# Kernel tuning notes

Hardware: AMD Instinct MI355X
Metric: run time of the kernel (lower is better)

The kernel has to match this reference:

```python
import jax, jax.numpy as jnp
import numpy as np

N_NODES = 131072
N_EDGES = 2097152
IN_DIM = 768
HID = 64
NODES_PER_GRAPH = 32
OUT_DIM = 2


def setup_inputs() -> dict:
    key = jax.random.key(0)
    k1, k2, k3, k4 = jax.random.split(key, 4)
    x = jax.random.normal(k1, (N_NODES, IN_DIM), dtype=jnp.float32)
    edge_index = jax.random.randint(k2, (2, N_EDGES), 0, N_NODES, dtype=jnp.int64)
    W_conv = jax.random.normal(k3, (IN_DIM, HID), dtype=jnp.float32) * 0.02
    b_conv = jnp.zeros((HID,), dtype=jnp.float32)
    W_lin = jax.random.normal(k4, (OUT_DIM, HID * NODES_PER_GRAPH), dtype=jnp.float32) * 0.02
    b_lin = jnp.zeros((OUT_DIM,), dtype=jnp.float32)
    return {"x": x, "edge_index": edge_index, "W_conv": W_conv,
            "b_conv": b_conv, "W_lin": W_lin, "b_lin": b_lin}


def reference(x, edge_index, W_conv, b_conv, W_lin, b_lin):
    N = x.shape[0]
    # GCNConv: add self-loops, symmetric normalization D^-1/2 (A+I) D^-1/2
    loops = jnp.arange(N, dtype=edge_index.dtype)
    src = jnp.concatenate([edge_index[0], loops])  # [E+N]
    dst = jnp.concatenate([edge_index[1], loops])
    deg = jax.ops.segment_sum(jnp.ones_like(dst, dtype=x.dtype), dst, num_segments=N)
    dinv = jax.lax.rsqrt(deg)  # deg >= 1 due to self-loops
    norm = dinv[src] * dinv[dst]  # [E+N]
    h = x @ W_conv  # [N, HID]
    msg = h[src] * norm[:, None]  # gather + scale
    out = jax.ops.segment_sum(msg, dst, num_segments=N) + b_conv  # scatter-add
    out = jax.nn.relu(out)
    out = out.reshape(-1, HID * NODES_PER_GRAPH)  # [B, 2048]
    logits = out @ W_lin.T + b_lin  # [B, OUT_DIM]
    return jax.nn.log_softmax(logits, axis=1)
```

## Files before the change

### kernel.cpp

```cpp
#include <hip/hip_runtime.h>
#include <hip/hip_bf16.h>

#define N_NODES 131072
#define N_EDGES 2097152
#define IN_DIM 768
#define HID 64
#define NPG 32
#define NGRAPH (N_NODES / NPG)

#define BM 128
#define GEMM_BLOCKS (N_NODES / BM)

#define RNG 128
#define NB (N_NODES / RNG)
#define EPB 4096
#define NCB (N_EDGES / EPB)
#define PBLK 8
#define RPB (NCB / PBLK)
#define PREP_BLK 192

typedef __attribute__((ext_vector_type(8))) short bf16x8;
typedef __attribute__((ext_vector_type(4))) float f32x4;

static __device__ __forceinline__ unsigned short f2bf(float f) {
    __hip_bfloat16 h = __float2bfloat16(f);
    return *reinterpret_cast<unsigned short*>(&h);
}
static __device__ __forceinline__ float bf2f(unsigned short s) {
    return __uint_as_float(((unsigned int)s) << 16);
}

__global__ __launch_bounds__(256) void gcn_prep_count(const float* __restrict__ W,
                                                      unsigned short* __restrict__ Wt,
                                                      const int* __restrict__ dst,
                                                      unsigned int* __restrict__ C) {
    __shared__ unsigned int hist[NB];
    int tid = threadIdx.x;
    if (blockIdx.x < PREP_BLK) {
        int i = blockIdx.x * 256 + tid;
        if (i < IN_DIM * HID) {
            int k = i >> 6, n = i & 63;
            Wt[n * IN_DIM + k] = f2bf(W[i]);
        }
        return;
    }
    int cb = blockIdx.x - PREP_BLK;
    for (int t = tid; t < NB; t += 256) hist[t] = 0u;
    __syncthreads();
    int base = cb * EPB;
    #pragma unroll
    for (int u = 0; u < EPB / 256; ++u) {
        int d = dst[base + u * 256 + tid];
        atomicAdd(&hist[d >> 7], 1u);
    }
    __syncthreads();
    for (int t = tid; t < NB; t += 256) C[(size_t)cb * NB + t] = hist[t];
}

__global__ __launch_bounds__(256) void gcn_prefA(unsigned int* __restrict__ C,
                                                 unsigned int* __restrict__ S) {
    int tid = threadIdx.x;
    int p = blockIdx.x;
    #pragma unroll
    for (int c = 0; c < 4; ++c) {
        int t = tid + c * 256;
        unsigned int run = 0;
        for (int r = 0; r < RPB; r += 8) {
            unsigned int v[8];
            size_t base = ((size_t)(p * RPB + r)) * NB + t;
            #pragma unroll
            for (int j = 0; j < 8; ++j) v[j] = C[base + (size_t)j * NB];
            #pragma unroll
            for (int j = 0; j < 8; ++j) { C[base + (size_t)j * NB] = run; run += v[j]; }
        }
        S[p * NB + t] = run;
    }
}

__global__ __launch_bounds__(256) void gcn_prefB(unsigned int* __restrict__ S,
                                                 unsigned int* __restrict__ bstart) {
    __shared__ unsigned int sm[256];
    int tid = threadIdx.x;
    unsigned int lexcl[4];
    unsigned int lrun = 0;
    #pragma unroll
    for (int j = 0; j < 4; ++j) {
        unsigned int t = tid * 4 + j;
        unsigned int r = 0;
        #pragma unroll
        for (int p = 0; p < PBLK; ++p) {
            unsigned int v = S[p * NB + t];
            S[p * NB + t] = r;
            r += v;
        }
        lexcl[j] = lrun;
        lrun += r;
    }
    sm[tid] = lrun;
    __syncthreads();
    for (int off = 1; off < 256; off <<= 1) {
        unsigned int u = (tid >= off) ? sm[tid - off] : 0u;
        __syncthreads();
        sm[tid] += u;
        __syncthreads();
    }
    unsigned int texcl = sm[tid] - lrun;
    #pragma unroll
    for (int j = 0; j < 4; ++j) bstart[tid * 4 + j] = texcl + lexcl[j];
    if (tid == 255) bstart[NB] = N_EDGES;
}

__global__ __launch_bounds__(256) void gcn_scatter(const int* __restrict__ src,
                                                   const int* __restrict__ dst,
                                                   const unsigned int* __restrict__ C,
                                                   const unsigned int* __restrict__ S,
                                                   const unsigned int* __restrict__ bstart,
                                                   unsigned int* __restrict__ part) {
    __shared__ unsigned int off[NB];
    int tid = threadIdx.x, cb = blockIdx.x;
    int p = cb >> 6;
    for (int t = tid; t < NB; t += 256)
        off[t] = bstart[t] + S[p * NB + t] + C[(size_t)cb * NB + t];
    __syncthreads();
    int base = cb * EPB;
    #pragma unroll
    for (int u = 0; u < EPB / 256; ++u) {
        int i = base + u * 256 + tid;
        int d = dst[i];
        unsigned int pos = atomicAdd(&off[d >> 7], 1u);
        part[pos] = (unsigned int)src[i] | ((unsigned int)(d & (RNG - 1)) << 17);
    }
}

__global__ __launch_bounds__(256) void gcn_sort2(const unsigned int* __restrict__ part,
                                                 const unsigned int* __restrict__ bstart,
                                                 unsigned int* __restrict__ part2,
                                                 unsigned int* __restrict__ nstart,
                                                 float* __restrict__ dinv) {
    __shared__ unsigned int hist[RNG];
    __shared__ unsigned int sc[RNG];
    __shared__ unsigned int off[RNG];
    int tid = threadIdx.x, b = blockIdx.x;
    if (tid < RNG) hist[tid] = 0u;
    __syncthreads();
    unsigned int s0 = bstart[b], s1 = bstart[b + 1];
    for (unsigned int j = s0 + tid; j < s1; j += 256)
        atomicAdd(&hist[part[j] >> 17], 1u);
    __syncthreads();
    if (tid < RNG) sc[tid] = hist[tid];
    __syncthreads();
    #pragma unroll
    for (int o = 1; o < RNG; o <<= 1) {
        unsigned int u = (tid < RNG && tid >= o) ? sc[tid - o] : 0u;
        __syncthreads();
        if (tid < RNG) sc[tid] += u;
        __syncthreads();
    }
    if (tid < RNG) {
        unsigned int excl = sc[tid] - hist[tid];
        nstart[b * RNG + tid] = s0 + excl;
        off[tid] = s0 + excl;
        dinv[b * RNG + tid] = rsqrtf((float)(hist[tid] + 1));
    }
    if (b == NB - 1 && tid == 0) nstart[N_NODES] = N_EDGES;
    __syncthreads();
    for (unsigned int j = s0 + tid; j < s1; j += 256) {
        unsigned int pr = part[j];
        unsigned int pos = atomicAdd(&off[pr >> 17], 1u);
        part2[pos] = pr & 0x1FFFF;
    }
}

__global__ __launch_bounds__(256) void gcn_gemm(const float* __restrict__ x,
                                                const unsigned short* __restrict__ Wt,
                                                const float* __restrict__ dinv,
                                                unsigned short* __restrict__ hsb) {
    int tid = threadIdx.x;
    int lane = tid & 63;
    int w = tid >> 6;
    int rowbase = blockIdx.x * BM;
    int rl = lane & 15;
    int kq = (lane >> 4) * 8;

    const float* xa0 = x + (size_t)(rowbase + w * 32 + rl) * IN_DIM + kq;
    const float* xa1 = xa0 + (size_t)16 * IN_DIM;
    const unsigned short* wp = Wt + (size_t)rl * IN_DIM + kq;

    f32x4 acc[2][4] = {};

    #pragma unroll 2
    for (int kb = 0; kb < IN_DIM; kb += 32) {
        f32x4 u0 = __builtin_nontemporal_load((const f32x4*)(xa0 + kb));
        f32x4 u1 = __builtin_nontemporal_load((const f32x4*)(xa0 + kb + 4));
        f32x4 u2 = __builtin_nontemporal_load((const f32x4*)(xa1 + kb));
        f32x4 u3 = __builtin_nontemporal_load((const f32x4*)(xa1 + kb + 4));
        bf16x8 b0 = *(const bf16x8*)(wp + kb);
        bf16x8 b1 = *(const bf16x8*)(wp + (size_t)16 * IN_DIM + kb);
        bf16x8 b2 = *(const bf16x8*)(wp + (size_t)32 * IN_DIM + kb);
        bf16x8 b3 = *(const bf16x8*)(wp + (size_t)48 * IN_DIM + kb);
        bf16x8 a0, a1;
        a0[0] = (short)f2bf(u0[0]); a0[1] = (short)f2bf(u0[1]);
        a0[2] = (short)f2bf(u0[2]); a0[3] = (short)f2bf(u0[3]);
        a0[4] = (short)f2bf(u1[0]); a0[5] = (short)f2bf(u1[1]);
        a0[6] = (short)f2bf(u1[2]); a0[7] = (short)f2bf(u1[3]);
        a1[0] = (short)f2bf(u2[0]); a1[1] = (short)f2bf(u2[1]);
        a1[2] = (short)f2bf(u2[2]); a1[3] = (short)f2bf(u2[3]);
        a1[4] = (short)f2bf(u3[0]); a1[5] = (short)f2bf(u3[1]);
        a1[6] = (short)f2bf(u3[2]); a1[7] = (short)f2bf(u3[3]);
        acc[0][0] = __builtin_amdgcn_mfma_f32_16x16x32_bf16(a0, b0, acc[0][0], 0, 0, 0);
        acc[1][0] = __builtin_amdgcn_mfma_f32_16x16x32_bf16(a1, b0, acc[1][0], 0, 0, 0);
        acc[0][1] = __builtin_amdgcn_mfma_f32_16x16x32_bf16(a0, b1, acc[0][1], 0, 0, 0);
        acc[1][1] = __builtin_amdgcn_mfma_f32_16x16x32_bf16(a1, b1, acc[1][1], 0, 0, 0);
        acc[0][2] = __builtin_amdgcn_mfma_f32_16x16x32_bf16(a0, b2, acc[0][2], 0, 0, 0);
        acc[1][2] = __builtin_amdgcn_mfma_f32_16x16x32_bf16(a1, b2, acc[1][2], 0, 0, 0);
        acc[0][3] = __builtin_amdgcn_mfma_f32_16x16x32_bf16(a0, b3, acc[0][3], 0, 0, 0);
        acc[1][3] = __builtin_amdgcn_mfma_f32_16x16x32_bf16(a1, b3, acc[1][3], 0, 0, 0);
    }
    #pragma unroll
    for (int rt = 0; rt < 2; ++rt) {
        int row0 = rowbase + w * 32 + rt * 16 + (lane >> 4) * 4;
        #pragma unroll
        for (int rr = 0; rr < 4; ++rr) {
            float dv = dinv[row0 + rr];
            #pragma unroll
            for (int ct = 0; ct < 4; ++ct) {
                int col = ct * 16 + rl;
                hsb[(size_t)(row0 + rr) * HID + col] = f2bf(acc[rt][ct][rr] * dv);
            }
        }
    }
}

__global__ __launch_bounds__(512) void gcn_agg(const unsigned short* __restrict__ hsb,
                                               const unsigned int* __restrict__ part2,
                                               const unsigned int* __restrict__ nstart,
                                               const float* __restrict__ dinv,
                                               const float* __restrict__ b_conv,
                                               const float* __restrict__ W_lin,
                                               const float* __restrict__ b_lin,
                                               float* __restrict__ out) {
    __shared__ float p0s[8], p1s[8];
    int tid = threadIdx.x, lane = tid & 63, w = tid >> 6;
    int g = blockIdx.x;
    float bc = b_conv[lane];
    float l0 = 0.f, l1 = 0.f;

    int i0 = g * NPG + w * 4;
    int cc[4];
    unsigned int stt[4];
    float dii[4];
    int sidx[4];
    float av[4];
    #pragma unroll
    for (int k = 0; k < 4; ++k) {
        int i = i0 + k;
        unsigned int st = nstart[i], en = nstart[i + 1];
        stt[k] = st;
        cc[k] = (int)(en - st);
        dii[k] = dinv[i];
    }
    #pragma unroll
    for (int k = 0; k < 4; ++k)
        sidx[k] = (lane < cc[k]) ? (int)part2[stt[k] + lane] : (i0 + k);
    #pragma unroll
    for (int k = 0; k < 4; ++k)
        av[k] = bf2f(hsb[(size_t)(i0 + k) * HID + lane]);

    int cmax = max(max(cc[0], cc[1]), max(cc[2], cc[3]));
    int clim = min(cmax, 64);
    for (int e = 0; e < clim; e += 4) {
        float v[4][4];
        #pragma unroll
        for (int k = 0; k < 4; ++k) {
            #pragma unroll
            for (int j = 0; j < 4; ++j) {
                int idx = e + j;
                int cl = idx < cc[k] ? idx : 0;
                int s = __shfl(sidx[k], cl);
                v[k][j] = bf2f(hsb[(size_t)s * HID + lane]);
            }
        }
        #pragma unroll
        for (int k = 0; k < 4; ++k) {
            #pragma unroll
            for (int j = 0; j < 4; ++j)
                if (e + j < cc[k]) av[k] += v[k][j];
        }
    }
    #pragma unroll
    for (int k = 0; k < 4; ++k)
        for (int e2 = 64; e2 < cc[k]; ++e2)
            av[k] += bf2f(hsb[(size_t)part2[stt[k] + e2] * HID + lane]);

    #pragma unroll
    for (int k = 0; k < 4; ++k) {
        int node = w * 4 + k;
        float v = fmaxf(fmaf(av[k], dii[k], bc), 0.f);
        l0 = fmaf(v, W_lin[node * HID + lane], l0);
        l1 = fmaf(v, W_lin[HID * NPG + node * HID + lane], l1);
    }
    #pragma unroll
    for (int d = 32; d > 0; d >>= 1) {
        l0 += __shfl_down(l0, d);
        l1 += __shfl_down(l1, d);
    }
    if (lane == 0) { p0s[w] = l0; p1s[w] = l1; }
    __syncthreads();
    if (tid == 0) {
        float A = b_lin[0], B = b_lin[1];
        #pragma unroll
        for (int j = 0; j < 8; ++j) { A += p0s[j]; B += p1s[j]; }
        float m = fmaxf(A, B);
        float lse = m + logf(expf(A - m) + expf(B - m));
        out[g * 2 + 0] = A - lse;
        out[g * 2 + 1] = B - lse;
    }
}

extern "C" void kernel_launch(void* const* d_in, const int* in_sizes, int n_in,
                              void* d_out, int out_size, void* d_ws, size_t ws_size,
                              hipStream_t stream) {
    const float* x  = (const float*)d_in[0];
    const int* ei   = (const int*)d_in[1];
    const float* Wc = (const float*)d_in[2];
    const float* bc = (const float*)d_in[3];
    const float* Wl = (const float*)d_in[4];
    const float* bl = (const float*)d_in[5];
    float* out = (float*)d_out;

    char* ws = (char*)d_ws;
    unsigned short* Wt   = (unsigned short*)(ws);
    float*          dinv = (float*)(ws + (128 << 10));
    unsigned int*  bstart= (unsigned int*)(ws + (640 << 10));
    unsigned int*  S     = (unsigned int*)(ws + (656 << 10));
    unsigned int*  part2 = (unsigned int*)(ws + (1u << 20));
    unsigned int*  nstart= (unsigned int*)(ws + (9u << 20));
    unsigned int*  C     = (unsigned int*)(ws + (10u << 20));
    unsigned int*  part  = (unsigned int*)(ws + (12u << 20));
    unsigned short* hsb  = (unsigned short*)(ws + (10u << 20));

    const int* srcIdx = ei;
    const int* dstIdx = ei + N_EDGES;

    gcn_prep_count<<<PREP_BLK + NCB, 256, 0, stream>>>(Wc, Wt, dstIdx, C);
    gcn_prefA<<<PBLK, 256, 0, stream>>>(C, S);
    gcn_prefB<<<1, 256, 0, stream>>>(S, bstart);
    gcn_scatter<<<NCB, 256, 0, stream>>>(srcIdx, dstIdx, C, S, bstart, part);
    gcn_sort2<<<NB, 256, 0, stream>>>(part, bstart, part2, nstart, dinv);
    gcn_gemm<<<GEMM_BLOCKS, 256, 0, stream>>>(x, Wt, dinv, hsb);
    gcn_agg<<<NGRAPH, 512, 0, stream>>>(hsb, part2, nstart, dinv, bc, Wl, bl, out);
}
```

Before: 262.4 us.

## Stage GEMM x tiles through LDS with swizzled direct global-to-LDS loads

The GEMM now copies each 128x32 fp32 x tile into shared memory using global_load_lds 16-byte transfers with an XOR swizzle, then reads the MFMA operands from LDS instead of issuing strided per-lane global loads. The goal is fully coalesced row reads of x, which dominates memory traffic. In exchange it adds two block barriers per k-step with no double buffering, which serializes load and compute and drops the prior unroll and nontemporal hints.

```diff
diff --git a/kernel.cpp b/kernel.cpp
--- a/kernel.cpp
+++ b/kernel.cpp
@@ -9,6 +9,7 @@
 #define NGRAPH (N_NODES / NPG)
 
 #define BM 128
+#define KC 32
 #define GEMM_BLOCKS (N_NODES / BM)
 
 #define RNG 128
@@ -28,6 +29,12 @@
 }
 static __device__ __forceinline__ float bf2f(unsigned short s) {
     return __uint_as_float(((unsigned int)s) << 16);
+}
+
+static __device__ __forceinline__ void gload_lds16(const float* g, float* l) {
+    __builtin_amdgcn_global_load_lds(
+        (const __attribute__((address_space(1))) void*)g,
+        (__attribute__((address_space(3))) void*)l, 16, 0, 0);
 }
 
 __global__ __launch_bounds__(256) void gcn_prep_count(const float* __restrict__ W,
@@ -175,6 +182,7 @@
                                                 const unsigned short* __restrict__ Wt,
                                                 const float* __restrict__ dinv,
                                                 unsigned short* __restrict__ hsb) {
+    __shared__ __align__(16) float xs[BM][KC];
     int tid = threadIdx.x;
     int lane = tid & 63;
     int w = tid >> 6;
@@ -182,31 +190,43 @@
     int rl = lane & 15;
     int kq = (lane >> 4) * 8;
 
-    const float* xa0 = x + (size_t)(rowbase + w * 32 + rl) * IN_DIM + kq;
-    const float* xa1 = xa0 + (size_t)16 * IN_DIM;
+    int jhi = lane >> 3, jlo = lane & 7;
+    int cg = jlo ^ jhi;
+    const float* gbase = x + (size_t)rowbase * IN_DIM + cg * 4;
     const unsigned short* wp = Wt + (size_t)rl * IN_DIM + kq;
 
+    int r0 = w * 32 + rl, r1 = r0 + 16;
+    int swz = rl & 7;
+    int G0 = (lane >> 4) * 2;
+    const float4* xsf = (const float4*)xs;
+
     f32x4 acc[2][4] = {};
 
-    #pragma unroll 2
-    for (int kb = 0; kb < IN_DIM; kb += 32) {
-        f32x4 u0 = __builtin_nontemporal_load((const f32x4*)(xa0 + kb));
-        f32x4 u1 = __builtin_nontemporal_load((const f32x4*)(xa0 + kb + 4));
-        f32x4 u2 = __builtin_nontemporal_load((const f32x4*)(xa1 + kb));
-        f32x4 u3 = __builtin_nontemporal_load((const f32x4*)(xa1 + kb + 4));
+    for (int kb = 0; kb < IN_DIM; kb += KC) {
+        #pragma unroll
+        for (int q = 0; q < 4; ++q) {
+            int segq = w * 4 + q;
+            const float* g = gbase + (size_t)(segq * 8 + jhi) * IN_DIM + kb;
+            gload_lds16(g, &xs[segq * 8][0]);
+        }
+        __syncthreads();
+        float4 p0 = xsf[r0 * 8 + (G0 ^ swz)];
+        float4 p1 = xsf[r0 * 8 + ((G0 + 1) ^ swz)];
+        float4 p2 = xsf[r1 * 8 + (G0 ^ swz)];
+        float4 p3 = xsf[r1 * 8 + ((G0 + 1) ^ swz)];
         bf16x8 b0 = *(const bf16x8*)(wp + kb);
         bf16x8 b1 = *(const bf16x8*)(wp + (size_t)16 * IN_DIM + kb);
         bf16x8 b2 = *(const bf16x8*)(wp + (size_t)32 * IN_DIM + kb);
         bf16x8 b3 = *(const bf16x8*)(wp + (size_t)48 * IN_DIM + kb);
         bf16x8 a0, a1;
-        a0[0] = (short)f2bf(u0[0]); a0[1] = (short)f2bf(u0[1]);
-        a0[2] = (short)f2bf(u0[2]); a0[3] = (short)f2bf(u0[3]);
-        a0[4] = (short)f2bf(u1[0]); a0[5] = (short)f2bf(u1[1]);
-        a0[6] = (short)f2bf(u1[2]); a0[7] = (short)f2bf(u1[3]);
-        a1[0] = (short)f2bf(u2[0]); a1[1] = (short)f2bf(u2[1]);
-        a1[2] = (short)f2bf(u2[2]); a1[3] = (short)f2bf(u2[3]);
-        a1[4] = (short)f2bf(u3[0]); a1[5] = (short)f2bf(u3[1]);
-        a1[6] = (short)f2bf(u3[2]); a1[7] = (short)f2bf(u3[3]);
+        a0[0] = (short)f2bf(p0.x); a0[1] = (short)f2bf(p0.y);
+        a0[2] = (short)f2bf(p0.z); a0[3] = (short)f2bf(p0.w);
+        a0[4] = (short)f2bf(p1.x); a0[5] = (short)f2bf(p1.y);
+        a0[6] = (short)f2bf(p1.z); a0[7] = (short)f2bf(p1.w);
+        a1[0] = (short)f2bf(p2.x); a1[1] = (short)f2bf(p2.y);
+        a1[2] = (short)f2bf(p2.z); a1[3] = (short)f2bf(p2.w);
+        a1[4] = (short)f2bf(p3.x); a1[5] = (short)f2bf(p3.y);
+        a1[6] = (short)f2bf(p3.z); a1[7] = (short)f2bf(p3.w);
         acc[0][0] = __builtin_amdgcn_mfma_f32_16x16x32_bf16(a0, b0, acc[0][0], 0, 0, 0);
         acc[1][0] = __builtin_amdgcn_mfma_f32_16x16x32_bf16(a1, b0, acc[1][0], 0, 0, 0);
         acc[0][1] = __builtin_amdgcn_mfma_f32_16x16x32_bf16(a0, b1, acc[0][1], 0, 0, 0);
@@ -215,6 +235,7 @@
         acc[1][2] = __builtin_amdgcn_mfma_f32_16x16x32_bf16(a1, b2, acc[1][2], 0, 0, 0);
         acc[0][3] = __builtin_amdgcn_mfma_f32_16x16x32_bf16(a0, b3, acc[0][3], 0, 0, 0);
         acc[1][3] = __builtin_amdgcn_mfma_f32_16x16x32_bf16(a1, b3, acc[1][3], 0, 0, 0);
+        __syncthreads();
     }
     #pragma unroll
     for (int rt = 0; rt < 2; ++rt) {
```

Result: faster. 232.3 us (-11.5%).
